# Optimization experiments

Measured on AMD Instinct MI355X. Metric: run time of the kernel, lower is better.

The kernel has to match this reference:

```python
import jax, jax.numpy as jnp
import numpy as np

N_CODES = 1024
DIM = 64
COMMITMENT = 0.25


def setup_inputs() -> dict:
    key = jax.random.key(0)
    k1, k2 = jax.random.split(key)
    z = jax.random.normal(k1, (32, DIM, 64, 64), dtype=jnp.float32)
    # nn.Embedding weight initialized uniform(-1/n_codes, 1/n_codes)
    codebook = jax.random.uniform(
        k2, (N_CODES, DIM), dtype=jnp.float32,
        minval=-1.0 / N_CODES, maxval=1.0 / N_CODES)
    return {"z": z, "codebook": codebook}


def reference(z, codebook):
    B, C, H, W = z.shape
    # (B,C,H,W) -> (B*H*W, C)
    z_flat = jnp.transpose(z, (0, 2, 3, 1)).reshape(-1, C)
    # squared L2 distances via expansion: |z|^2 + |e|^2 - 2 z.e
    dists = (
        jnp.sum(z_flat ** 2, axis=1, keepdims=True)
        + jnp.sum(codebook ** 2, axis=1)
        - 2.0 * z_flat @ codebook.T
    )  # [N, n_codes]
    indices = jnp.argmin(dists, axis=1)  # [N]
    z_q = jnp.transpose(codebook[indices].reshape(B, H, W, C), (0, 3, 1, 2))
    commit_loss = jnp.mean((jax.lax.stop_gradient(z_q) - z) ** 2)
    codebook_loss = jnp.mean((z_q - jax.lax.stop_gradient(z)) ** 2)
    vq_loss = codebook_loss + COMMITMENT * commit_loss
    z_q_st = z + jax.lax.stop_gradient(z_q - z)  # straight-through
    return (z_q_st, vq_loss)
```

## Files before the change

### kernel.cpp

```cpp
#include <hip/hip_runtime.h>


constexpr int DIM    = 64;
constexpr int NCODES = 1024;
constexpr int HWSZ   = 4096;
constexpr int NPOS   = 131072;
constexpr int BLOCK  = 1024;
constexpr int PPB    = 256;
constexpr int GRID   = NPOS / PPB;

typedef float    f32x4  __attribute__((ext_vector_type(4)));
typedef float    f32x2  __attribute__((ext_vector_type(2)));
typedef unsigned uint2v __attribute__((ext_vector_type(2)));
typedef unsigned uint4v __attribute__((ext_vector_type(4)));

__global__ __launch_bounds__(256) void vq_prep(const float* __restrict__ cb,
                                               float* __restrict__ cinitT,
                                               unsigned* __restrict__ cbq) {
    int j = blockIdx.x * 256 + threadIdx.x;
    const float4* src = (const float4*)(cb + (size_t)j * DIM);
    unsigned words[16];
    float nq = 0.f;
#pragma unroll
    for (int g8 = 0; g8 < 8; g8++) {
        float4 v0 = src[g8 * 2], v1 = src[g8 * 2 + 1];
        int lo = 0, hi = 0;
        lo = __builtin_amdgcn_cvt_pk_fp8_f32(v0.x * 512.f, v0.y * 512.f, lo, 0);
        lo = __builtin_amdgcn_cvt_pk_fp8_f32(v0.z * 512.f, v0.w * 512.f, lo, 1);
        hi = __builtin_amdgcn_cvt_pk_fp8_f32(v1.x * 512.f, v1.y * 512.f, hi, 0);
        hi = __builtin_amdgcn_cvt_pk_fp8_f32(v1.z * 512.f, v1.w * 512.f, hi, 1);
        words[g8 * 2] = (unsigned)lo; words[g8 * 2 + 1] = (unsigned)hi;
#pragma unroll
        for (int m = 0; m < 2; m++) {
            int wv = m ? hi : lo;
            f32x2 d0 = __builtin_amdgcn_cvt_pk_f32_fp8(wv, 0);
            f32x2 d1 = __builtin_amdgcn_cvt_pk_f32_fp8(wv, 1);
            nq += d0[0] * d0[0] + d0[1] * d0[1] + d1[0] * d1[0] + d1[1] * d1[1];
        }
    }
#pragma unroll
    for (int u = 0; u < 4; u++) {
        int us = u ^ (j & 3);
        uint4v t = {words[2 * u], words[2 * u + 1],
                    words[2 * u + 8], words[2 * u + 9]};
        *(uint4v*)(cbq + (size_t)j * 16 + us * 4) = t;
    }
    cinitT[(j & 15) * 64 + (j >> 4)] = 8.f - nq * (1.f / 1024.f);
}

__global__ __launch_bounds__(BLOCK, 8) void vq_main(const float* __restrict__ z,
                                                    const float* __restrict__ cinitT,
                                                    const unsigned* __restrict__ cbq,
                                                    float* __restrict__ out,
                                                    float* __restrict__ wsblk) {
    __shared__ __align__(16) unsigned char cb_lds[NCODES * DIM];
    __shared__ int   bj_lds[PPB];
    __shared__ float ls_lds[BLOCK / 64];

    const int tid  = threadIdx.x;
    const int w    = tid >> 6;
    const int lane = tid & 63;
    const int q    = lane >> 4;
    const int r    = lane & 15;
    const int p0   = blockIdx.x * PPB;
    const int b    = p0 >> 12;
    const int hwb  = p0 & 4095;

#pragma unroll
    for (int it = 0; it < (NCODES * DIM) / (BLOCK * 16); it++) {
        int off = (it * BLOCK + tid) * 16;
        __builtin_amdgcn_global_load_lds(
            (const __attribute__((address_space(1))) void*)((const char*)cbq + off),
            (__attribute__((address_space(3))) void*)(cb_lds + off), 16, 0, 0);
    }

    long  afrag[2];
    float zsq;
    {
        const float* zb = z + (size_t)b * DIM * HWSZ + hwb + w * 16 + r;
        float sq = 0.f;
#pragma unroll
        for (int h = 0; h < 2; h++) {
            float v[8];
#pragma unroll
            for (int i = 0; i < 8; i++) {
                v[i] = zb[(size_t)(h * 32 + q * 8 + i) * HWSZ];
                sq = fmaf(v[i], v[i], sq);
            }
            int lo = 0, hi = 0;
            lo = __builtin_amdgcn_cvt_pk_fp8_f32(v[0], v[1], lo, 0);
            lo = __builtin_amdgcn_cvt_pk_fp8_f32(v[2], v[3], lo, 1);
            hi = __builtin_amdgcn_cvt_pk_fp8_f32(v[4], v[5], hi, 0);
            hi = __builtin_amdgcn_cvt_pk_fp8_f32(v[6], v[7], hi, 1);
            uint2v u = {(unsigned)lo, (unsigned)hi};
            afrag[h] = __builtin_bit_cast(long, u);
        }
        sq += __shfl_xor(sq, 16, 64);
        sq += __shfl_xor(sq, 32, 64);
        zsq = sq;
    }

    __syncthreads();

    const int bbase = r * 64 + ((q ^ (r & 3)) * 16);

    float best[4];
#pragma unroll
    for (int g = 0; g < 4; g++) best[g] = 0.f;
    float tmp[4];

    uint4v Bp[2];
    Bp[0] = *(const uint4v*)&cb_lds[0 * 1024 + bbase];
    Bp[1] = *(const uint4v*)&cb_lds[1 * 1024 + bbase];
    float4 ci[2];
    ci[0] = *(const float4*)(cinitT + r * 64 + 0);
    ci[1] = *(const float4*)(cinitT + r * 64 + 4);

#pragma unroll
    for (int G = 0; G < 16; G++) {
#pragma unroll
        for (int e = 0; e < 4; e++) {
            const int jt   = G * 4 + e;
            const int slot = jt & 1;
            const int row  = jt * 16;
            const float cin = ci[G & 1][e];
            const unsigned inv_j = (unsigned)(1023 - row);
            uint2v blo = {Bp[slot][0], Bp[slot][1]};
            uint2v bhi = {Bp[slot][2], Bp[slot][3]};
            f32x4 c0 = {cin, cin, cin, cin};
            f32x4 acc = __builtin_amdgcn_mfma_f32_16x16x32_fp8_fp8(
                afrag[0], __builtin_bit_cast(long, blo), c0, 0, 0, 0);
            acc = __builtin_amdgcn_mfma_f32_16x16x32_fp8_fp8(
                afrag[1], __builtin_bit_cast(long, bhi), acc, 0, 0, 0);
#pragma unroll
            for (int g = 0; g < 4; g++) {
                unsigned bits = (__float_as_uint(acc[g]) & ~1023u)
                              | (inv_j - (unsigned)r);
                float pf = __uint_as_float(bits);
                if ((jt & 1) == 0) {
                    tmp[g] = pf;
                } else {
                    best[g] = fmaxf(fmaxf(best[g], tmp[g]), pf);
                }
            }
            Bp[slot] = *(const uint4v*)&cb_lds[(((jt + 2) & 63) * 1024) + bbase];
        }
        ci[G & 1] = *(const float4*)(cinitT + r * 64 + (((G + 2) & 15) * 4));
    }

    unsigned bestu[4];
#pragma unroll
    for (int g = 0; g < 4; g++) {
        unsigned v = __float_as_uint(best[g]);
#pragma unroll
        for (int off = 1; off < 16; off <<= 1) {
            unsigned v2 = __shfl_xor((int)v, off, 64);
            v = v > v2 ? v : v2;
        }
        bestu[g] = v;
    }

    float lsum = 0.f;
    if (q == (r >> 2)) {
        int g = r & 3;
        unsigned v = bestu[0];
        v = (g == 1) ? bestu[1] : v;
        v = (g == 2) ? bestu[2] : v;
        v = (g == 3) ? bestu[3] : v;
        bj_lds[w * 16 + r] = 1023 - (int)(v & 1023u);
        lsum = zsq + (8.f - __uint_as_float(v)) * (1.f / 256.f);
    }
#pragma unroll
    for (int off = 32; off > 0; off >>= 1) lsum += __shfl_down(lsum, off, 64);
    if (lane == 0) ls_lds[w] = lsum;
    __syncthreads();
    if (tid == 0) {
        float s = 0.f;
#pragma unroll
        for (int i = 0; i < BLOCK / 64; i++) s += ls_lds[i];
        wsblk[blockIdx.x] = s;
    }

    int posi = tid & 255;
    int u    = tid >> 8;
    int myj  = bj_lds[posi];
    int us   = u ^ (myj & 3);
    uint4v t = *(const uint4v*)&cb_lds[(size_t)myj * 64 + us * 16];
    float* ob = out + (size_t)b * DIM * HWSZ + hwb + posi;
#pragma unroll
    for (int m = 0; m < 2; m++) {
        int cbase = (m == 0) ? (8 * u) : (32 + 8 * u);
#pragma unroll
        for (int wd = 0; wd < 2; wd++) {
            int word = (int)t[m * 2 + wd];
            f32x2 d0 = __builtin_amdgcn_cvt_pk_f32_fp8(word, 0);
            f32x2 d1 = __builtin_amdgcn_cvt_pk_f32_fp8(word, 1);
            ob[(size_t)(cbase + wd * 4 + 0) * HWSZ] = d0[0] * (1.f / 512.f);
            ob[(size_t)(cbase + wd * 4 + 1) * HWSZ] = d0[1] * (1.f / 512.f);
            ob[(size_t)(cbase + wd * 4 + 2) * HWSZ] = d1[0] * (1.f / 512.f);
            ob[(size_t)(cbase + wd * 4 + 3) * HWSZ] = d1[1] * (1.f / 512.f);
        }
    }
}

__global__ void vq_fin(const float* __restrict__ wsblk, float* __restrict__ out_loss) {
    int t = threadIdx.x;
    float s = 0.f;
#pragma unroll
    for (int k = 0; k < GRID / 64; k++) s += wsblk[t + k * 64];
#pragma unroll
    for (int off = 32; off > 0; off >>= 1) s += __shfl_down(s, off, 64);
    if (t == 0) out_loss[0] = 1.25f * s / (float)((size_t)NPOS * DIM);
}

extern "C" void kernel_launch(void* const* d_in, const int* in_sizes, int n_in,
                              void* d_out, int out_size, void* d_ws, size_t ws_size,
                              hipStream_t stream) {
    const float* z  = (const float*)d_in[0];
    const float* cb = (const float*)d_in[1];
    float* out = (float*)d_out;

    float*    cinitT = (float*)d_ws;
    unsigned* cbq    = (unsigned*)((char*)d_ws + 4096);
    float*    wsblk  = (float*)((char*)d_ws + 4096 + 65536);

    vq_prep<<<NCODES / 256, 256, 0, stream>>>(cb, cinitT, cbq);
    vq_main<<<GRID, BLOCK, 0, stream>>>(z, cinitT, cbq, out, wsblk);
    vq_fin<<<1, 64, 0, stream>>>(wsblk, out + (size_t)NPOS * DIM);
}
```

Before: 107.1 us.

## Fuse codebook quantization and loss reduction into single main kernel

```diff
diff --git a/kernel.cpp b/kernel.cpp
--- a/kernel.cpp
+++ b/kernel.cpp
@@ -8,52 +8,18 @@
 constexpr int BLOCK  = 1024;
 constexpr int PPB    = 256;
 constexpr int GRID   = NPOS / PPB;
+constexpr int CIP    = 68;
 
 typedef float    f32x4  __attribute__((ext_vector_type(4)));
 typedef float    f32x2  __attribute__((ext_vector_type(2)));
 typedef unsigned uint2v __attribute__((ext_vector_type(2)));
 typedef unsigned uint4v __attribute__((ext_vector_type(4)));
 
-__global__ __launch_bounds__(256) void vq_prep(const float* __restrict__ cb,
-                                               float* __restrict__ cinitT,
-                                               unsigned* __restrict__ cbq) {
-    int j = blockIdx.x * 256 + threadIdx.x;
-    const float4* src = (const float4*)(cb + (size_t)j * DIM);
-    unsigned words[16];
-    float nq = 0.f;
-#pragma unroll
-    for (int g8 = 0; g8 < 8; g8++) {
-        float4 v0 = src[g8 * 2], v1 = src[g8 * 2 + 1];
-        int lo = 0, hi = 0;
-        lo = __builtin_amdgcn_cvt_pk_fp8_f32(v0.x * 512.f, v0.y * 512.f, lo, 0);
-        lo = __builtin_amdgcn_cvt_pk_fp8_f32(v0.z * 512.f, v0.w * 512.f, lo, 1);
-        hi = __builtin_amdgcn_cvt_pk_fp8_f32(v1.x * 512.f, v1.y * 512.f, hi, 0);
-        hi = __builtin_amdgcn_cvt_pk_fp8_f32(v1.z * 512.f, v1.w * 512.f, hi, 1);
-        words[g8 * 2] = (unsigned)lo; words[g8 * 2 + 1] = (unsigned)hi;
-#pragma unroll
-        for (int m = 0; m < 2; m++) {
-            int wv = m ? hi : lo;
-            f32x2 d0 = __builtin_amdgcn_cvt_pk_f32_fp8(wv, 0);
-            f32x2 d1 = __builtin_amdgcn_cvt_pk_f32_fp8(wv, 1);
-            nq += d0[0] * d0[0] + d0[1] * d0[1] + d1[0] * d1[0] + d1[1] * d1[1];
-        }
-    }
-#pragma unroll
-    for (int u = 0; u < 4; u++) {
-        int us = u ^ (j & 3);
-        uint4v t = {words[2 * u], words[2 * u + 1],
-                    words[2 * u + 8], words[2 * u + 9]};
-        *(uint4v*)(cbq + (size_t)j * 16 + us * 4) = t;
-    }
-    cinitT[(j & 15) * 64 + (j >> 4)] = 8.f - nq * (1.f / 1024.f);
-}
-
-__global__ __launch_bounds__(BLOCK, 8) void vq_main(const float* __restrict__ z,
-                                                    const float* __restrict__ cinitT,
-                                                    const unsigned* __restrict__ cbq,
-                                                    float* __restrict__ out,
-                                                    float* __restrict__ wsblk) {
+__global__ __launch_bounds__(BLOCK, 8) void vq_all(const float* __restrict__ z,
+                                                   const float* __restrict__ cb,
+                                                   float* __restrict__ out) {
     __shared__ __align__(16) unsigned char cb_lds[NCODES * DIM];
+    __shared__ float cinit_lds[16 * CIP];
     __shared__ int   bj_lds[PPB];
     __shared__ float ls_lds[BLOCK / 64];
 
@@ -66,12 +32,37 @@
     const int b    = p0 >> 12;
     const int hwb  = p0 & 4095;
 
-#pragma unroll
-    for (int it = 0; it < (NCODES * DIM) / (BLOCK * 16); it++) {
-        int off = (it * BLOCK + tid) * 16;
-        __builtin_amdgcn_global_load_lds(
-            (const __attribute__((address_space(1))) void*)((const char*)cbq + off),
-            (__attribute__((address_space(3))) void*)(cb_lds + off), 16, 0, 0);
+    {
+        const int j = tid;
+        const float4* src = (const float4*)(cb + (size_t)j * DIM);
+        unsigned words[16];
+        float nq = 0.f;
+#pragma unroll
+        for (int g8 = 0; g8 < 8; g8++) {
+            float4 v0 = src[g8 * 2], v1 = src[g8 * 2 + 1];
+            int lo = 0, hi = 0;
+            lo = __builtin_amdgcn_cvt_pk_fp8_f32(v0.x * 512.f, v0.y * 512.f, lo, 0);
+            lo = __builtin_amdgcn_cvt_pk_fp8_f32(v0.z * 512.f, v0.w * 512.f, lo, 1);
+            hi = __builtin_amdgcn_cvt_pk_fp8_f32(v1.x * 512.f, v1.y * 512.f, hi, 0);
+            hi = __builtin_amdgcn_cvt_pk_fp8_f32(v1.z * 512.f, v1.w * 512.f, hi, 1);
+            words[g8 * 2] = (unsigned)lo; words[g8 * 2 + 1] = (unsigned)hi;
+#pragma unroll
+            for (int m = 0; m < 2; m++) {
+                int wv = m ? hi : lo;
+                f32x2 d0 = __builtin_amdgcn_cvt_pk_f32_fp8(wv, 0);
+                f32x2 d1 = __builtin_amdgcn_cvt_pk_f32_fp8(wv, 1);
+                nq += d0[0] * d0[0] + d0[1] * d0[1] + d1[0] * d1[0] + d1[1] * d1[1];
+            }
+        }
+        const int sswz = (j & 3) ^ ((j >> 2) & 1);
+#pragma unroll
+        for (int u = 0; u < 4; u++) {
+            int us = u ^ sswz;
+            uint4v tq = {words[2 * u], words[2 * u + 1],
+                         words[2 * u + 8], words[2 * u + 9]};
+            *(uint4v*)&cb_lds[(size_t)j * 64 + us * 16] = tq;
+        }
+        cinit_lds[(j & 15) * CIP + (j >> 4)] = 8.f - nq * (1.f / 1024.f);
     }
 
     long  afrag[2];
@@ -102,7 +93,7 @@
 
     __syncthreads();
 
-    const int bbase = r * 64 + ((q ^ (r & 3)) * 16);
+    const int bbase = r * 64 + ((q ^ (r & 3) ^ ((r >> 2) & 1)) * 16);
 
     float best[4];
 #pragma unroll
@@ -113,8 +104,8 @@
     Bp[0] = *(const uint4v*)&cb_lds[0 * 1024 + bbase];
     Bp[1] = *(const uint4v*)&cb_lds[1 * 1024 + bbase];
     float4 ci[2];
-    ci[0] = *(const float4*)(cinitT + r * 64 + 0);
-    ci[1] = *(const float4*)(cinitT + r * 64 + 4);
+    ci[0] = *(const float4*)&cinit_lds[r * CIP + 0];
+    ci[1] = *(const float4*)&cinit_lds[r * CIP + 4];
 
 #pragma unroll
     for (int G = 0; G < 16; G++) {
@@ -145,7 +136,7 @@
             }
             Bp[slot] = *(const uint4v*)&cb_lds[(((jt + 2) & 63) * 1024) + bbase];
         }
-        ci[G & 1] = *(const float4*)(cinitT + r * 64 + (((G + 2) & 15) * 4));
+        ci[G & 1] = *(const float4*)&cinit_lds[r * CIP + (((G + 2) & 15) * 4)];
     }
 
     unsigned bestu[4];
@@ -178,13 +169,13 @@
         float s = 0.f;
 #pragma unroll
         for (int i = 0; i < BLOCK / 64; i++) s += ls_lds[i];
-        wsblk[blockIdx.x] = s;
+        atomicAdd(out + (size_t)NPOS * DIM, s * (1.25f / 8388608.f));
     }
 
     int posi = tid & 255;
     int u    = tid >> 8;
     int myj  = bj_lds[posi];
-    int us   = u ^ (myj & 3);
+    int us   = u ^ (myj & 3) ^ ((myj >> 2) & 1);
     uint4v t = *(const uint4v*)&cb_lds[(size_t)myj * 64 + us * 16];
     float* ob = out + (size_t)b * DIM * HWSZ + hwb + posi;
 #pragma unroll
@@ -203,16 +194,6 @@
     }
 }
 
-__global__ void vq_fin(const float* __restrict__ wsblk, float* __restrict__ out_loss) {
-    int t = threadIdx.x;
-    float s = 0.f;
-#pragma unroll
-    for (int k = 0; k < GRID / 64; k++) s += wsblk[t + k * 64];
-#pragma unroll
-    for (int off = 32; off > 0; off >>= 1) s += __shfl_down(s, off, 64);
-    if (t == 0) out_loss[0] = 1.25f * s / (float)((size_t)NPOS * DIM);
-}
-
 extern "C" void kernel_launch(void* const* d_in, const int* in_sizes, int n_in,
                               void* d_out, int out_size, void* d_ws, size_t ws_size,
                               hipStream_t stream) {
@@ -220,11 +201,6 @@
     const float* cb = (const float*)d_in[1];
     float* out = (float*)d_out;
 
-    float*    cinitT = (float*)d_ws;
-    unsigned* cbq    = (unsigned*)((char*)d_ws + 4096);
-    float*    wsblk  = (float*)((char*)d_ws + 4096 + 65536);
-
-    vq_prep<<<NCODES / 256, 256, 0, stream>>>(cb, cinitT, cbq);
-    vq_main<<<GRID, BLOCK, 0, stream>>>(z, cinitT, cbq, out, wsblk);
-    vq_fin<<<1, 64, 0, stream>>>(wsblk, out + (size_t)NPOS * DIM);
+    hipMemsetAsync(out + (size_t)NPOS * DIM, 0, sizeof(float), stream);
+    vq_all<<<GRID, BLOCK, 0, stream>>>(z, cb, out);
 }
```

After: 110.2 us. 1.03x slower.
